# Kernel optimization log

Hardware: AMD Instinct MI355X
Metric: run time of the kernel (lower is better)

Reference implementation:

```python
import jax, jax.numpy as jnp
import numpy as np

SLIDING_WINDOW = 2048
NUM_SINK = 4


def make_mask(q_len, k_len, dtype=jnp.float32):
    # positions of queries in the key axis
    q_pos = jnp.arange(k_len - q_len, k_len)[:, None]  # [Q,1]
    k_pos = jnp.arange(k_len)[None, :]                 # [1,K]
    causal = k_pos <= q_pos
    in_window = k_pos >= (q_pos - SLIDING_WINDOW + 1)
    is_sink = k_pos < NUM_SINK
    allowed = causal & (in_window | is_sink)
    return jnp.where(allowed, jnp.zeros((), dtype), jnp.full((), -jnp.inf, dtype))


def setup_inputs() -> dict:
    key = jax.random.key(0)
    k1, k2, k3 = jax.random.split(key, 3)
    B, H, L, D = 2, 16, 4096, 128
    q = jax.random.normal(k1, (B, H, L, D), dtype=jnp.float32)
    k = jax.random.normal(k2, (B, H, L, D), dtype=jnp.float32)
    v = jax.random.normal(k3, (B, H, L, D), dtype=jnp.float32)
    return {"q": q, "k": k, "v": v}


def reference(q, k, v):
    B, H, L, D = q.shape
    mask = make_mask(L, k.shape[2], q.dtype)  # [L, L] additive
    scale = 1.0 / jnp.sqrt(jnp.asarray(D, q.dtype))
    scores = jnp.einsum('bhqd,bhkd->bhqk', q, k) * scale + mask
    probs = jax.nn.softmax(scores, axis=-1)
    return jnp.einsum('bhqk,bhkd->bhqd', probs, v)
```

## Files before the change

kernel.cpp:

```cpp
#include <hip/hip_runtime.h>

constexpr int Ld = 4096;
constexpr int Dd = 128;
constexpr int BQ = 128;
constexpr int BK = 64;
constexpr int WSZ = 2048;
constexpr int NSINK = 4;
constexpr float QSCALE = 0.08838834764831845f * 1.4426950408889634f;

typedef short bf16x8 __attribute__((ext_vector_type(8)));
typedef float f32x4 __attribute__((ext_vector_type(4)));

#if defined(__has_builtin)
#if __has_builtin(__builtin_amdgcn_exp2f)
#define EXP2(x) __builtin_amdgcn_exp2f(x)
#endif
#endif
#ifndef EXP2
#define EXP2(x) exp2f(x)
#endif

__device__ __forceinline__ unsigned pkbf(float hi, float lo) {
    unsigned r;
    asm("v_cvt_pk_bf16_f32 %0, %1, %2" : "=v"(r) : "v"(lo), "v"(hi));
    return r;
}

__device__ __forceinline__ int rd_off(int row, int d) {
    return row * 128 + ((((d >> 3) ^ row) & 15) << 3) + (d & 7);
}
__device__ __forceinline__ int vt_off(int drow, int key) {
    return drow * 64 + ((((key >> 3) ^ drow) & 7) << 3) + (key & 7);
}
__device__ __forceinline__ int p_off(int row, int key) {
    return row * 64 + ((((key >> 2) ^ ((row & 7) << 1)) & 15) << 2) + (key & 3);
}

typedef const __attribute__((address_space(1))) unsigned int* gas1_t;
typedef __attribute__((address_space(3))) unsigned int* las3_t;
__device__ __forceinline__ void lds16(const void* g, void* l) {
    __builtin_amdgcn_global_load_lds((gas1_t)g, (las3_t)l, 16, 0, 0);
}

__global__ __launch_bounds__(256)
void cvt_kv(const float* __restrict__ Kg, const float* __restrict__ Vg,
            unsigned short* __restrict__ Kw, unsigned short* __restrict__ Vw) {
    __shared__ __align__(16) unsigned short vt[8192];
    const int tid = threadIdx.x;
    const int kb = blockIdx.x * BK;
    const int bh = blockIdx.y;
    const size_t gbase = ((size_t)bh * Ld + kb) * Dd;

    #pragma unroll
    for (int i = 0; i < 8; ++i) {
        int id = tid + i * 256;
        int row = id >> 5;
        int d0 = (id & 31) << 2;
        float4 a = *(const float4*)(Kg + gbase + (size_t)row * Dd + d0);
        *(uint2*)&Kw[gbase + rd_off(row, d0)] =
            make_uint2(pkbf(a.y, a.x), pkbf(a.w, a.z));
    }

    const int vd  = tid & 127;
    const int vkh = tid >> 7;
    const float* vp = Vg + gbase + (size_t)vkh * 32 * Dd + vd;
    float vr[32];
    #pragma unroll
    for (int j = 0; j < 32; ++j) vr[j] = vp[(size_t)j * Dd];
    #pragma unroll
    for (int m2 = 0; m2 < 4; ++m2)
        *(uint4*)&vt[vt_off(vd, vkh * 32 + m2 * 8)] =
            make_uint4(pkbf(vr[m2 * 8 + 1], vr[m2 * 8 + 0]),
                       pkbf(vr[m2 * 8 + 3], vr[m2 * 8 + 2]),
                       pkbf(vr[m2 * 8 + 5], vr[m2 * 8 + 4]),
                       pkbf(vr[m2 * 8 + 7], vr[m2 * 8 + 6]));
    __syncthreads();
    const size_t vbase = ((size_t)bh * (Ld / BK) + blockIdx.x) * (size_t)(BK * Dd);
    #pragma unroll
    for (int i = 0; i < 4; ++i) {
        int j = tid + i * 256;
        *(uint4*)&Vw[vbase + (size_t)j * 8] = *(const uint4*)&vt[j * 8];
    }
}

__global__ __launch_bounds__(256, 3)
void swa_fwd2(const float* __restrict__ Qg, const unsigned short* __restrict__ Kw,
              const unsigned short* __restrict__ Vw, float* __restrict__ Og) {
    __shared__ __align__(16) unsigned short smem[24576];
    unsigned short* Vts = smem + 8192;
    unsigned short* Ps  = smem + 16384;
    unsigned short* Qst = smem;

    const int tid  = threadIdx.x;
    const int w    = tid >> 6;
    const int lane = tid & 63;
    const int ml   = lane & 15;
    const int quad = lane >> 4;

    const unsigned wgr = blockIdx.x;
    const unsigned nwg = gridDim.x;
    unsigned wgid = wgr;
    if ((nwg & 7u) == 0u) wgid = (wgr & 7u) * (nwg >> 3) + (wgr >> 3);
    const int tpb   = Ld / BQ;
    const int bh    = (int)(wgid / (unsigned)tpb);
    const int qtile = tpb - 1 - (int)(wgid % (unsigned)tpb);
    const int q0 = qtile * BQ;

    const size_t baseQ = ((size_t)bh * Ld + q0) * Dd;

    #pragma unroll
    for (int i = 0; i < 16; ++i) {
        int idx = tid + i * 256;
        int row = idx >> 5;
        int d0  = (idx & 31) << 2;
        float4 v = *(const float4*)(Qg + baseQ + (size_t)row * Dd + d0);
        *(uint2*)&Qst[rd_off(row, d0)] =
            make_uint2(pkbf(v.y * QSCALE, v.x * QSCALE),
                       pkbf(v.w * QSCALE, v.z * QSCALE));
    }
    __syncthreads();

    bf16x8 qf[2][4];
    #pragma unroll
    for (int g = 0; g < 2; ++g)
        #pragma unroll
        for (int k0 = 0; k0 < 4; ++k0)
            qf[g][k0] = *(const bf16x8*)&Qst[rd_off(w * 32 + g * 16 + ml,
                                                    k0 * 32 + quad * 8)];
    __syncthreads();

    float l_i[2] = {0.f, 0.f};
    f32x4 o_acc[2][8];
    #pragma unroll
    for (int g = 0; g < 2; ++g)
        #pragma unroll
        for (int dt = 0; dt < 8; ++dt)
            o_acc[g][dt] = (f32x4){0.f, 0.f, 0.f, 0.f};

    const int kmin = (q0 - (WSZ - 1)) > 0 ? (q0 - (WSZ - 1)) : 0;
    const int kb_first = (kmin / BK) * BK;
    const bool sink_extra = (kb_first > 0);
    const int nch = (q0 + BQ - kb_first) / BK + (sink_extra ? 1 : 0);

    const int qrow0 = q0 + w * 32 + ml;
    unsigned short* Pw = Ps + w * 2048;

    auto kb_of = [&](int ci) {
        return sink_extra ? (ci == 0 ? 0 : kb_first + (ci - 1) * BK)
                          : kb_first + ci * BK;
    };
    const size_t kwbase = (size_t)bh * Ld * Dd;
    const size_t vwbase = (size_t)bh * (Ld / BK) * (size_t)(BK * Dd);

    auto stageK = [&](int ci) {
        const int kb = kb_of(ci);
        const unsigned short* kg = Kw + kwbase + (size_t)kb * Dd + tid * 8;
        unsigned short* kl = smem + tid * 8;
        #pragma unroll
        for (int i = 0; i < 4; ++i) lds16(kg + i * 2048, kl + i * 2048);
    };
    auto stageV = [&](int ci) {
        const int kb = kb_of(ci);
        const unsigned short* vg = Vw + vwbase + (size_t)(kb >> 6) * (BK * Dd) + tid * 8;
        unsigned short* vl = Vts + tid * 8;
        #pragma unroll
        for (int i = 0; i < 4; ++i) lds16(vg + i * 2048, vl + i * 2048);
    };

    stageK(0);

    for (int ci = 0; ci < nch; ++ci) {
        __syncthreads();
        stageV(ci);

        const int kb = kb_of(ci);
        const int ck = (ci + 1 < nch) ? ci + 1 : ci;

        f32x4 s[2][4];
        #pragma unroll
        for (int g = 0; g < 2; ++g)
            #pragma unroll
            for (int t = 0; t < 4; ++t)
                s[g][t] = (f32x4){0.f, 0.f, 0.f, 0.f};
        __builtin_amdgcn_s_setprio(1);
        #pragma unroll
        for (int k0 = 0; k0 < 4; ++k0) {
            bf16x8 ka[4];
            #pragma unroll
            for (int t = 0; t < 4; ++t)
                ka[t] = *(const bf16x8*)&smem[rd_off(t * 16 + ml, k0 * 32 + quad * 8)];
            #pragma unroll
            for (int t = 0; t < 4; ++t) {
                s[0][t] = __builtin_amdgcn_mfma_f32_16x16x32_bf16(ka[t], qf[0][k0], s[0][t], 0, 0, 0);
                s[1][t] = __builtin_amdgcn_mfma_f32_16x16x32_bf16(ka[t], qf[1][k0], s[1][t], 0, 0, 0);
            }
        }
        __builtin_amdgcn_s_setprio(0);

        asm volatile("s_waitcnt lgkmcnt(0)" ::: "memory");
        __builtin_amdgcn_sched_barrier(0);
        __builtin_amdgcn_s_barrier();
        stageK(ck);

        const bool full = (kb + (BK - 1) <= q0) && (kb >= q0 + BQ - WSZ);

        #pragma unroll
        for (int g = 0; g < 2; ++g) {
            const int q = qrow0 + g * 16;
            if (!full) {
                #pragma unroll
                for (int t = 0; t < 4; ++t)
                    #pragma unroll
                    for (int r = 0; r < 4; ++r) {
                        int k = kb + t * 16 + quad * 4 + r;
                        bool ok = (k <= q) && ((k + (WSZ - 1) >= q) || (k < NSINK));
                        s[g][t][r] = ok ? s[g][t][r] : -3e38f;
                    }
            }
            float rs = 0.f;
            #pragma unroll
            for (int t = 0; t < 4; ++t)
                #pragma unroll
                for (int r = 0; r < 4; ++r) {
                    float p = EXP2(s[g][t][r]);
                    s[g][t][r] = p;
                    rs += p;
                }
            l_i[g] += rs;

            unsigned short* Pg = Pw + g * 1024;
            #pragma unroll
            for (int t = 0; t < 4; ++t)
                *(uint2*)&Pg[p_off(ml, t * 16 + quad * 4)] =
                    make_uint2(pkbf(s[g][t][1], s[g][t][0]),
                               pkbf(s[g][t][3], s[g][t][2]));
        }

        asm volatile("s_waitcnt vmcnt(4)" ::: "memory");
        __builtin_amdgcn_sched_barrier(0);
        __builtin_amdgcn_s_barrier();

        __builtin_amdgcn_s_setprio(1);
        #pragma unroll
        for (int k0 = 0; k0 < 2; ++k0) {
            bf16x8 pb0 = *(const bf16x8*)&Pw[p_off(ml, k0 * 32 + quad * 8)];
            bf16x8 pb1 = *(const bf16x8*)&Pw[1024 + p_off(ml, k0 * 32 + quad * 8)];
            #pragma unroll
            for (int dt = 0; dt < 8; ++dt) {
                bf16x8 va = *(const bf16x8*)&Vts[vt_off(dt * 16 + ml, k0 * 32 + quad * 8)];
                o_acc[0][dt] = __builtin_amdgcn_mfma_f32_16x16x32_bf16(va, pb0, o_acc[0][dt], 0, 0, 0);
                o_acc[1][dt] = __builtin_amdgcn_mfma_f32_16x16x32_bf16(va, pb1, o_acc[1][dt], 0, 0, 0);
            }
        }
        __builtin_amdgcn_s_setprio(0);
    }

    #pragma unroll
    for (int g = 0; g < 2; ++g) {
        float lt = l_i[g];
        lt += __shfl_xor(lt, 16);
        lt += __shfl_xor(lt, 32);
        const float inv = 1.f / lt;
        float* op = Og + ((size_t)bh * Ld + (qrow0 + g * 16)) * Dd;
        #pragma unroll
        for (int dt = 0; dt < 8; ++dt) {
            float4 o;
            o.x = o_acc[g][dt][0] * inv;
            o.y = o_acc[g][dt][1] * inv;
            o.z = o_acc[g][dt][2] * inv;
            o.w = o_acc[g][dt][3] * inv;
            *(float4*)(op + dt * 16 + quad * 4) = o;
        }
    }
}

__global__ __launch_bounds__(256, 2)
void swa_fwd(const float* __restrict__ Qg, const float* __restrict__ Kg,
             const float* __restrict__ Vg, float* __restrict__ Og) {
    __shared__ __align__(16) unsigned short smem[24576];
    unsigned short* Ks  = smem;
    unsigned short* Vts = smem + 8192;
    unsigned short* Ps  = smem + 16384;
    unsigned short* Qst = smem;

    const int tid  = threadIdx.x;
    const int w    = tid >> 6;
    const int lane = tid & 63;
    const int ml   = lane & 15;
    const int quad = lane >> 4;

    const int qtile = (int)(gridDim.x - 1u - blockIdx.x);
    const int q0 = qtile * BQ;
    const int bh = blockIdx.y;

    const size_t baseQ  = ((size_t)bh * Ld + q0) * Dd;
    const size_t baseKV = (size_t)bh * Ld * Dd;

    #pragma unroll
    for (int i = 0; i < 16; ++i) {
        int idx = tid + i * 256;
        int row = idx >> 5;
        int d0  = (idx & 31) << 2;
        float4 v = *(const float4*)(Qg + baseQ + (size_t)row * Dd + d0);
        *(uint2*)&Qst[rd_off(row, d0)] =
            make_uint2(pkbf(v.y * QSCALE, v.x * QSCALE),
                       pkbf(v.w * QSCALE, v.z * QSCALE));
    }
    __syncthreads();

    bf16x8 qf[2][4];
    #pragma unroll
    for (int g = 0; g < 2; ++g)
        #pragma unroll
        for (int k0 = 0; k0 < 4; ++k0)
            qf[g][k0] = *(const bf16x8*)&Qst[rd_off(w * 32 + g * 16 + ml,
                                                    k0 * 32 + quad * 8)];

    float l_i[2] = {0.f, 0.f};
    f32x4 o_acc[2][8];
    #pragma unroll
    for (int g = 0; g < 2; ++g)
        #pragma unroll
        for (int dt = 0; dt < 8; ++dt)
            o_acc[g][dt] = (f32x4){0.f, 0.f, 0.f, 0.f};

    const int kmin = (q0 - (WSZ - 1)) > 0 ? (q0 - (WSZ - 1)) : 0;
    const int kb_first = (kmin / BK) * BK;
    const bool sink_extra = (kb_first > 0);
    const int nch = (q0 + BQ - kb_first) / BK + (sink_extra ? 1 : 0);

    const int qrow0 = q0 + w * 32 + ml;
    unsigned short* Pw = Ps + w * 2048;

    float4 kreg[8];
    float  vreg[32];
    const int kr0 = tid >> 5;
    const int kd0 = (tid & 31) << 2;
    const int vd  = tid & 127;
    const int vkh = tid >> 7;

    auto kvload = [&](int kb) {
        const float* kp = Kg + baseKV + (size_t)(kb + kr0) * Dd + kd0;
        #pragma unroll
        for (int i = 0; i < 8; ++i)
            kreg[i] = *(const float4*)(kp + (size_t)i * 8 * Dd);
        const float* vp = Vg + baseKV + (size_t)(kb + vkh * 32) * Dd + vd;
        #pragma unroll
        for (int j = 0; j < 32; ++j)
            vreg[j] = vp[(size_t)j * Dd];
    };
    auto kb_of = [&](int ci) {
        return sink_extra ? (ci == 0 ? 0 : kb_first + (ci - 1) * BK)
                          : kb_first + ci * BK;
    };

    kvload(kb_of(0));

    for (int ci = 0; ci < nch; ++ci) {
        const int kb = kb_of(ci);
        __syncthreads();
        #pragma unroll
        for (int i = 0; i < 8; ++i)
            *(uint2*)&Ks[rd_off(kr0 + i * 8, kd0)] =
                make_uint2(pkbf(kreg[i].y, kreg[i].x),
                           pkbf(kreg[i].w, kreg[i].z));
        #pragma unroll
        for (int m2 = 0; m2 < 4; ++m2) {
            *(uint4*)&Vts[vt_off(vd, vkh * 32 + m2 * 8)] =
                make_uint4(pkbf(vreg[m2 * 8 + 1], vreg[m2 * 8 + 0]),
                           pkbf(vreg[m2 * 8 + 3], vreg[m2 * 8 + 2]),
                           pkbf(vreg[m2 * 8 + 5], vreg[m2 * 8 + 4]),
                           pkbf(vreg[m2 * 8 + 7], vreg[m2 * 8 + 6]));
        }
        __syncthreads();
        if (ci + 1 < nch) kvload(kb_of(ci + 1));

        f32x4 s[2][4];
        #pragma unroll
        for (int g = 0; g < 2; ++g)
            #pragma unroll
            for (int t = 0; t < 4; ++t)
                s[g][t] = (f32x4){0.f, 0.f, 0.f, 0.f};
        #pragma unroll
        for (int k0 = 0; k0 < 4; ++k0) {
            bf16x8 ka[4];
            #pragma unroll
            for (int t = 0; t < 4; ++t)
                ka[t] = *(const bf16x8*)&Ks[rd_off(t * 16 + ml, k0 * 32 + quad * 8)];
            #pragma unroll
            for (int t = 0; t < 4; ++t) {
                s[0][t] = __builtin_amdgcn_mfma_f32_16x16x32_bf16(ka[t], qf[0][k0], s[0][t], 0, 0, 0);
                s[1][t] = __builtin_amdgcn_mfma_f32_16x16x32_bf16(ka[t], qf[1][k0], s[1][t], 0, 0, 0);
            }
        }

        const bool full = (kb + (BK - 1) <= q0) && (kb >= q0 + BQ - WSZ);

        #pragma unroll
        for (int g = 0; g < 2; ++g) {
            const int q = qrow0 + g * 16;
            if (!full) {
                #pragma unroll
                for (int t = 0; t < 4; ++t)
                    #pragma unroll
                    for (int r = 0; r < 4; ++r) {
                        int k = kb + t * 16 + quad * 4 + r;
                        bool ok = (k <= q) && ((k + (WSZ - 1) >= q) || (k < NSINK));
                        s[g][t][r] = ok ? s[g][t][r] : -3e38f;
                    }
            }
            float rs = 0.f;
            #pragma unroll
            for (int t = 0; t < 4; ++t)
                #pragma unroll
                for (int r = 0; r < 4; ++r) {
                    float p = EXP2(s[g][t][r]);
                    s[g][t][r] = p;
                    rs += p;
                }
            l_i[g] += rs;

            unsigned short* Pg = Pw + g * 1024;
            #pragma unroll
            for (int t = 0; t < 4; ++t)
                *(uint2*)&Pg[p_off(ml, t * 16 + quad * 4)] =
                    make_uint2(pkbf(s[g][t][1], s[g][t][0]),
                               pkbf(s[g][t][3], s[g][t][2]));
        }

        #pragma unroll
        for (int k0 = 0; k0 < 2; ++k0) {
            bf16x8 pb0 = *(const bf16x8*)&Pw[p_off(ml, k0 * 32 + quad * 8)];
            bf16x8 pb1 = *(const bf16x8*)&Pw[1024 + p_off(ml, k0 * 32 + quad * 8)];
            #pragma unroll
            for (int dt = 0; dt < 8; ++dt) {
                bf16x8 va = *(const bf16x8*)&Vts[vt_off(dt * 16 + ml, k0 * 32 + quad * 8)];
                o_acc[0][dt] = __builtin_amdgcn_mfma_f32_16x16x32_bf16(va, pb0, o_acc[0][dt], 0, 0, 0);
                o_acc[1][dt] = __builtin_amdgcn_mfma_f32_16x16x32_bf16(va, pb1, o_acc[1][dt], 0, 0, 0);
            }
        }
    }

    #pragma unroll
    for (int g = 0; g < 2; ++g) {
        float lt = l_i[g];
        lt += __shfl_xor(lt, 16);
        lt += __shfl_xor(lt, 32);
        const float inv = 1.f / lt;
        float* op = Og + ((size_t)bh * Ld + (qrow0 + g * 16)) * Dd;
        #pragma unroll
        for (int dt = 0; dt < 8; ++dt) {
            float4 o;
            o.x = o_acc[g][dt][0] * inv;
            o.y = o_acc[g][dt][1] * inv;
            o.z = o_acc[g][dt][2] * inv;
            o.w = o_acc[g][dt][3] * inv;
            *(float4*)(op + dt * 16 + quad * 4) = o;
        }
    }
}

extern "C" void kernel_launch(void* const* d_in, const int* in_sizes, int n_in,
                              void* d_out, int out_size, void* d_ws, size_t ws_size,
                              hipStream_t stream) {
    const float* q = (const float*)d_in[0];
    const float* k = (const float*)d_in[1];
    const float* v = (const float*)d_in[2];
    float* o = (float*)d_out;
    const int bhn = in_sizes[0] / (Ld * Dd);
    const size_t elems = (size_t)bhn * Ld * Dd;
    const size_t need = 2 * elems * sizeof(unsigned short);
    if (d_ws != nullptr && ws_size >= need) {
        unsigned short* Kw = (unsigned short*)d_ws;
        unsigned short* Vw = Kw + elems;
        cvt_kv<<<dim3(Ld / BK, bhn), dim3(256, 1, 1), 0, stream>>>(k, v, Kw, Vw);
        swa_fwd2<<<dim3((unsigned)(bhn * (Ld / BQ))), dim3(256, 1, 1), 0, stream>>>(q, Kw, Vw, o);
    } else {
        dim3 grid(Ld / BQ, bhn);
        swa_fwd<<<grid, dim3(256, 1, 1), 0, stream>>>(q, k, v, o);
    }
}
```

Measured before the change: 351.2 us.

## Process 128-key chunks per iteration with two-half QK/PV interleave

Doubles the key chunk handled per loop iteration from 64 to 128 keys. The V-conversion kernel now writes V in a 128-key transposed, swizzled layout, and LDS grows to hold 128-key K and V tiles. Each iteration computes QK and softmax for two 64-key halves, then runs two PV passes, which halves the number of barrier and staging rounds. In exchange, LDS use rises, occupancy drops from 3 to 2 blocks per CU, and the sink chunk wastes half of a 128-key load.

```diff
diff --git a/kernel.cpp b/kernel.cpp
--- a/kernel.cpp
+++ b/kernel.cpp
@@ -4,6 +4,7 @@
 constexpr int Dd = 128;
 constexpr int BQ = 128;
 constexpr int BK = 64;
+constexpr int CHK = 128;
 constexpr int WSZ = 2048;
 constexpr int NSINK = 4;
 constexpr float QSCALE = 0.08838834764831845f * 1.4426950408889634f;
@@ -29,8 +30,11 @@
 __device__ __forceinline__ int rd_off(int row, int d) {
     return row * 128 + ((((d >> 3) ^ row) & 15) << 3) + (d & 7);
 }
-__device__ __forceinline__ int vt_off(int drow, int key) {
+__device__ __forceinline__ int vt64(int drow, int key) {
     return drow * 64 + ((((key >> 3) ^ drow) & 7) << 3) + (key & 7);
+}
+__device__ __forceinline__ int vt128(int drow, int key) {
+    return drow * 128 + ((((key >> 3) ^ drow) & 15) << 3) + (key & 7);
 }
 __device__ __forceinline__ int p_off(int row, int key) {
     return row * 64 + ((((key >> 2) ^ ((row & 7) << 1)) & 15) << 2) + (key & 3);
@@ -69,26 +73,32 @@
     for (int j = 0; j < 32; ++j) vr[j] = vp[(size_t)j * Dd];
     #pragma unroll
     for (int m2 = 0; m2 < 4; ++m2)
-        *(uint4*)&vt[vt_off(vd, vkh * 32 + m2 * 8)] =
+        *(uint4*)&vt[vt64(vd, vkh * 32 + m2 * 8)] =
             make_uint4(pkbf(vr[m2 * 8 + 1], vr[m2 * 8 + 0]),
                        pkbf(vr[m2 * 8 + 3], vr[m2 * 8 + 2]),
                        pkbf(vr[m2 * 8 + 5], vr[m2 * 8 + 4]),
                        pkbf(vr[m2 * 8 + 7], vr[m2 * 8 + 6]));
     __syncthreads();
-    const size_t vbase = ((size_t)bh * (Ld / BK) + blockIdx.x) * (size_t)(BK * Dd);
+    const int t128 = kb >> 7;
+    const int khalf = (kb >> 6) & 1;
+    const size_t vbase = (size_t)bh * Ld * Dd + (size_t)t128 * (CHK * Dd);
     #pragma unroll
     for (int i = 0; i < 4; ++i) {
         int j = tid + i * 256;
-        *(uint4*)&Vw[vbase + (size_t)j * 8] = *(const uint4*)&vt[j * 8];
-    }
-}
-
-__global__ __launch_bounds__(256, 3)
+        int d = j >> 3;
+        int kb8 = j & 7;
+        *(uint4*)&Vw[vbase + d * 128 +
+                     ((((khalf * 8 + kb8) ^ d) & 15) << 3)] =
+            *(const uint4*)&vt[vt64(d, kb8 * 8)];
+    }
+}
+
+__global__ __launch_bounds__(256, 2)
 void swa_fwd2(const float* __restrict__ Qg, const unsigned short* __restrict__ Kw,
               const unsigned short* __restrict__ Vw, float* __restrict__ Og) {
-    __shared__ __align__(16) unsigned short smem[24576];
-    unsigned short* Vts = smem + 8192;
-    unsigned short* Ps  = smem + 16384;
+    __shared__ __align__(16) unsigned short smem[40960];
+    unsigned short* Vts = smem + 16384;
+    unsigned short* Ps  = smem + 32768;
     unsigned short* Qst = smem;
 
     const int tid  = threadIdx.x;
@@ -138,45 +148,36 @@
             o_acc[g][dt] = (f32x4){0.f, 0.f, 0.f, 0.f};
 
     const int kmin = (q0 - (WSZ - 1)) > 0 ? (q0 - (WSZ - 1)) : 0;
-    const int kb_first = (kmin / BK) * BK;
+    const int kb_first = (kmin / CHK) * CHK;
     const bool sink_extra = (kb_first > 0);
-    const int nch = (q0 + BQ - kb_first) / BK + (sink_extra ? 1 : 0);
+    const int nch = (q0 + BQ - kb_first) / CHK + (sink_extra ? 1 : 0);
 
     const int qrow0 = q0 + w * 32 + ml;
     unsigned short* Pw = Ps + w * 2048;
 
     auto kb_of = [&](int ci) {
-        return sink_extra ? (ci == 0 ? 0 : kb_first + (ci - 1) * BK)
-                          : kb_first + ci * BK;
+        return sink_extra ? (ci == 0 ? 0 : kb_first + (ci - 1) * CHK)
+                          : kb_first + ci * CHK;
     };
     const size_t kwbase = (size_t)bh * Ld * Dd;
-    const size_t vwbase = (size_t)bh * (Ld / BK) * (size_t)(BK * Dd);
+    const size_t vwbase = (size_t)bh * Ld * Dd;
 
     auto stageK = [&](int ci) {
         const int kb = kb_of(ci);
         const unsigned short* kg = Kw + kwbase + (size_t)kb * Dd + tid * 8;
         unsigned short* kl = smem + tid * 8;
         #pragma unroll
-        for (int i = 0; i < 4; ++i) lds16(kg + i * 2048, kl + i * 2048);
+        for (int i = 0; i < 8; ++i) lds16(kg + i * 2048, kl + i * 2048);
     };
     auto stageV = [&](int ci) {
         const int kb = kb_of(ci);
-        const unsigned short* vg = Vw + vwbase + (size_t)(kb >> 6) * (BK * Dd) + tid * 8;
+        const unsigned short* vg = Vw + vwbase + (size_t)(kb >> 7) * (CHK * Dd) + tid * 8;
         unsigned short* vl = Vts + tid * 8;
         #pragma unroll
-        for (int i = 0; i < 4; ++i) lds16(vg + i * 2048, vl + i * 2048);
-    };
-
-    stageK(0);
-
-    for (int ci = 0; ci < nch; ++ci) {
-        __syncthreads();
-        stageV(ci);
-
-        const int kb = kb_of(ci);
-        const int ck = (ci + 1 < nch) ? ci + 1 : ci;
-
-        f32x4 s[2][4];
+        for (int i = 0; i < 8; ++i) lds16(vg + i * 2048, vl + i * 2048);
+    };
+
+    auto qk_half = [&](int h, f32x4 (&s)[2][4]) {
         #pragma unroll
         for (int g = 0; g < 2; ++g)
             #pragma unroll
@@ -188,7 +189,8 @@
             bf16x8 ka[4];
             #pragma unroll
             for (int t = 0; t < 4; ++t)
-                ka[t] = *(const bf16x8*)&smem[rd_off(t * 16 + ml, k0 * 32 + quad * 8)];
+                ka[t] = *(const bf16x8*)&smem[rd_off(h * 64 + t * 16 + ml,
+                                                     k0 * 32 + quad * 8)];
             #pragma unroll
             for (int t = 0; t < 4; ++t) {
                 s[0][t] = __builtin_amdgcn_mfma_f32_16x16x32_bf16(ka[t], qf[0][k0], s[0][t], 0, 0, 0);
@@ -196,11 +198,239 @@
             }
         }
         __builtin_amdgcn_s_setprio(0);
+    };
+
+    auto softmax_half = [&](int h, int kb, f32x4 (&s)[2][4]) {
+        const bool fullh = (kb + h * 64 + 63 <= q0) &&
+                           (kb + h * 64 >= q0 + BQ - WSZ);
+        #pragma unroll
+        for (int g = 0; g < 2; ++g) {
+            const int q = qrow0 + g * 16;
+            if (!fullh) {
+                #pragma unroll
+                for (int t = 0; t < 4; ++t)
+                    #pragma unroll
+                    for (int r = 0; r < 4; ++r) {
+                        int k = kb + h * 64 + t * 16 + quad * 4 + r;
+                        bool ok = (k <= q) && ((k + (WSZ - 1) >= q) || (k < NSINK));
+                        s[g][t][r] = ok ? s[g][t][r] : -3e38f;
+                    }
+            }
+            float rs = 0.f;
+            #pragma unroll
+            for (int t = 0; t < 4; ++t)
+                #pragma unroll
+                for (int r = 0; r < 4; ++r) {
+                    float p = EXP2(s[g][t][r]);
+                    s[g][t][r] = p;
+                    rs += p;
+                }
+            l_i[g] += rs;
+        }
+    };
+
+    auto storeP = [&](f32x4 (&s)[2][4]) {
+        #pragma unroll
+        for (int g = 0; g < 2; ++g) {
+            unsigned short* Pg = Pw + g * 1024;
+            #pragma unroll
+            for (int t = 0; t < 4; ++t)
+                *(uint2*)&Pg[p_off(ml, t * 16 + quad * 4)] =
+                    make_uint2(pkbf(s[g][t][1], s[g][t][0]),
+                               pkbf(s[g][t][3], s[g][t][2]));
+        }
+    };
+
+    auto pv_half = [&](int h) {
+        __builtin_amdgcn_s_setprio(1);
+        #pragma unroll
+        for (int k0 = 0; k0 < 2; ++k0) {
+            bf16x8 pb0 = *(const bf16x8*)&Pw[p_off(ml, k0 * 32 + quad * 8)];
+            bf16x8 pb1 = *(const bf16x8*)&Pw[1024 + p_off(ml, k0 * 32 + quad * 8)];
+            #pragma unroll
+            for (int dt = 0; dt < 8; ++dt) {
+                bf16x8 va = *(const bf16x8*)&Vts[vt128(dt * 16 + ml,
+                                                       h * 64 + k0 * 32 + quad * 8)];
+                o_acc[0][dt] = __builtin_amdgcn_mfma_f32_16x16x32_bf16(va, pb0, o_acc[0][dt], 0, 0, 0);
+                o_acc[1][dt] = __builtin_amdgcn_mfma_f32_16x16x32_bf16(va, pb1, o_acc[1][dt], 0, 0, 0);
+            }
+        }
+        __builtin_amdgcn_s_setprio(0);
+    };
+
+    stageK(0);
+
+    for (int ci = 0; ci < nch; ++ci) {
+        __syncthreads();
+        stageV(ci);
+
+        const int kb = kb_of(ci);
+        const int ck = (ci + 1 < nch) ? ci + 1 : ci;
+        const bool sinkch = sink_extra && (ci == 0);
+
+        f32x4 s0[2][4], s1[2][4];
+        qk_half(0, s0);
+        softmax_half(0, kb, s0);
+        storeP(s0);
+        if (!sinkch) {
+            qk_half(1, s1);
+            softmax_half(1, kb, s1);
+        }
 
         asm volatile("s_waitcnt lgkmcnt(0)" ::: "memory");
         __builtin_amdgcn_sched_barrier(0);
         __builtin_amdgcn_s_barrier();
         stageK(ck);
+
+        asm volatile("s_waitcnt vmcnt(8)" ::: "memory");
+        __builtin_amdgcn_sched_barrier(0);
+        __builtin_amdgcn_s_barrier();
+
+        pv_half(0);
+        if (!sinkch) {
+            storeP(s1);
+            pv_half(1);
+        }
+    }
+
+    #pragma unroll
+    for (int g = 0; g < 2; ++g) {
+        float lt = l_i[g];
+        lt += __shfl_xor(lt, 16);
+        lt += __shfl_xor(lt, 32);
+        const float inv = 1.f / lt;
+        float* op = Og + ((size_t)bh * Ld + (qrow0 + g * 16)) * Dd;
+        #pragma unroll
+        for (int dt = 0; dt < 8; ++dt) {
+            float4 o;
+            o.x = o_acc[g][dt][0] * inv;
+            o.y = o_acc[g][dt][1] * inv;
+            o.z = o_acc[g][dt][2] * inv;
+            o.w = o_acc[g][dt][3] * inv;
+            *(float4*)(op + dt * 16 + quad * 4) = o;
+        }
+    }
+}
+
+__global__ __launch_bounds__(256, 2)
+void swa_fwd(const float* __restrict__ Qg, const float* __restrict__ Kg,
+             const float* __restrict__ Vg, float* __restrict__ Og) {
+    __shared__ __align__(16) unsigned short smem[24576];
+    unsigned short* Ks  = smem;
+    unsigned short* Vts = smem + 8192;
+    unsigned short* Ps  = smem + 16384;
+    unsigned short* Qst = smem;
+
+    const int tid  = threadIdx.x;
+    const int w    = tid >> 6;
+    const int lane = tid & 63;
+    const int ml   = lane & 15;
+    const int quad = lane >> 4;
+
+    const int qtile = (int)(gridDim.x - 1u - blockIdx.x);
+    const int q0 = qtile * BQ;
+    const int bh = blockIdx.y;
+
+    const size_t baseQ  = ((size_t)bh * Ld + q0) * Dd;
+    const size_t baseKV = (size_t)bh * Ld * Dd;
+
+    #pragma unroll
+    for (int i = 0; i < 16; ++i) {
+        int idx = tid + i * 256;
+        int row = idx >> 5;
+        int d0  = (idx & 31) << 2;
+        float4 v = *(const float4*)(Qg + baseQ + (size_t)row * Dd + d0);
+        *(uint2*)&Qst[rd_off(row, d0)] =
+            make_uint2(pkbf(v.y * QSCALE, v.x * QSCALE),
+                       pkbf(v.w * QSCALE, v.z * QSCALE));
+    }
+    __syncthreads();
+
+    bf16x8 qf[2][4];
+    #pragma unroll
+    for (int g = 0; g < 2; ++g)
+        #pragma unroll
+        for (int k0 = 0; k0 < 4; ++k0)
+            qf[g][k0] = *(const bf16x8*)&Qst[rd_off(w * 32 + g * 16 + ml,
+                                                    k0 * 32 + quad * 8)];
+
+    float l_i[2] = {0.f, 0.f};
+    f32x4 o_acc[2][8];
+    #pragma unroll
+    for (int g = 0; g < 2; ++g)
+        #pragma unroll
+        for (int dt = 0; dt < 8; ++dt)
+            o_acc[g][dt] = (f32x4){0.f, 0.f, 0.f, 0.f};
+
+    const int kmin = (q0 - (WSZ - 1)) > 0 ? (q0 - (WSZ - 1)) : 0;
+    const int kb_first = (kmin / BK) * BK;
+    const bool sink_extra = (kb_first > 0);
+    const int nch = (q0 + BQ - kb_first) / BK + (sink_extra ? 1 : 0);
+
+    const int qrow0 = q0 + w * 32 + ml;
+    unsigned short* Pw = Ps + w * 2048;
+
+    float4 kreg[8];
+    float  vreg[32];
+    const int kr0 = tid >> 5;
+    const int kd0 = (tid & 31) << 2;
+    const int vd  = tid & 127;
+    const int vkh = tid >> 7;
+
+    auto kvload = [&](int kb) {
+        const float* kp = Kg + baseKV + (size_t)(kb + kr0) * Dd + kd0;
+        #pragma unroll
+        for (int i = 0; i < 8; ++i)
+            kreg[i] = *(const float4*)(kp + (size_t)i * 8 * Dd);
+        const float* vp = Vg + baseKV + (size_t)(kb + vkh * 32) * Dd + vd;
+        #pragma unroll
+        for (int j = 0; j < 32; ++j)
+            vreg[j] = vp[(size_t)j * Dd];
+    };
+    auto kb_of = [&](int ci) {
+        return sink_extra ? (ci == 0 ? 0 : kb_first + (ci - 1) * BK)
+                          : kb_first + ci * BK;
+    };
+
+    kvload(kb_of(0));
+
+    for (int ci = 0; ci < nch; ++ci) {
+        const int kb = kb_of(ci);
+        __syncthreads();
+        #pragma unroll
+        for (int i = 0; i < 8; ++i)
+            *(uint2*)&Ks[rd_off(kr0 + i * 8, kd0)] =
+                make_uint2(pkbf(kreg[i].y, kreg[i].x),
+                           pkbf(kreg[i].w, kreg[i].z));
+        #pragma unroll
+        for (int m2 = 0; m2 < 4; ++m2) {
+            *(uint4*)&Vts[vt64(vd, vkh * 32 + m2 * 8)] =
+                make_uint4(pkbf(vreg[m2 * 8 + 1], vreg[m2 * 8 + 0]),
+                           pkbf(vreg[m2 * 8 + 3], vreg[m2 * 8 + 2]),
+                           pkbf(vreg[m2 * 8 + 5], vreg[m2 * 8 + 4]),
+                           pkbf(vreg[m2 * 8 + 7], vreg[m2 * 8 + 6]));
+        }
+        __syncthreads();
+        if (ci + 1 < nch) kvload(kb_of(ci + 1));
+
+        f32x4 s[2][4];
+        #pragma unroll
+        for (int g = 0; g < 2; ++g)
+            #pragma unroll
+            for (int t = 0; t < 4; ++t)
+                s[g][t] = (f32x4){0.f, 0.f, 0.f, 0.f};
+        #pragma unroll
+        for (int k0 = 0; k0 < 4; ++k0) {
+            bf16x8 ka[4];
+            #pragma unroll
+            for (int t = 0; t < 4; ++t)
+                ka[t] = *(const bf16x8*)&Ks[rd_off(t * 16 + ml, k0 * 32 + quad * 8)];
+            #pragma unroll
+            for (int t = 0; t < 4; ++t) {
+                s[0][t] = __builtin_amdgcn_mfma_f32_16x16x32_bf16(ka[t], qf[0][k0], s[0][t], 0, 0, 0);
+                s[1][t] = __builtin_amdgcn_mfma_f32_16x16x32_bf16(ka[t], qf[1][k0], s[1][t], 0, 0, 0);
+            }
+        }
 
         const bool full = (kb + (BK - 1) <= q0) && (kb >= q0 + BQ - WSZ);
 
@@ -236,205 +466,13 @@
                                pkbf(s[g][t][3], s[g][t][2]));
         }
 
-        asm volatile("s_waitcnt vmcnt(4)" ::: "memory");
-        __builtin_amdgcn_sched_barrier(0);
-        __builtin_amdgcn_s_barrier();
-
-        __builtin_amdgcn_s_setprio(1);
         #pragma unroll
         for (int k0 = 0; k0 < 2; ++k0) {
             bf16x8 pb0 = *(const bf16x8*)&Pw[p_off(ml, k0 * 32 + quad * 8)];
             bf16x8 pb1 = *(const bf16x8*)&Pw[1024 + p_off(ml, k0 * 32 + quad * 8)];
             #pragma unroll
             for (int dt = 0; dt < 8; ++dt) {
-                bf16x8 va = *(const bf16x8*)&Vts[vt_off(dt * 16 + ml, k0 * 32 + quad * 8)];
-                o_acc[0][dt] = __builtin_amdgcn_mfma_f32_16x16x32_bf16(va, pb0, o_acc[0][dt], 0, 0, 0);
-                o_acc[1][dt] = __builtin_amdgcn_mfma_f32_16x16x32_bf16(va, pb1, o_acc[1][dt], 0, 0, 0);
-            }
-        }
-        __builtin_amdgcn_s_setprio(0);
-    }
-
-    #pragma unroll
-    for (int g = 0; g < 2; ++g) {
-        float lt = l_i[g];
-        lt += __shfl_xor(lt, 16);
-        lt += __shfl_xor(lt, 32);
-        const float inv = 1.f / lt;
-        float* op = Og + ((size_t)bh * Ld + (qrow0 + g * 16)) * Dd;
-        #pragma unroll
-        for (int dt = 0; dt < 8; ++dt) {
-            float4 o;
-            o.x = o_acc[g][dt][0] * inv;
-            o.y = o_acc[g][dt][1] * inv;
-            o.z = o_acc[g][dt][2] * inv;
-            o.w = o_acc[g][dt][3] * inv;
-            *(float4*)(op + dt * 16 + quad * 4) = o;
-        }
-    }
-}
-
-__global__ __launch_bounds__(256, 2)
-void swa_fwd(const float* __restrict__ Qg, const float* __restrict__ Kg,
-             const float* __restrict__ Vg, float* __restrict__ Og) {
-    __shared__ __align__(16) unsigned short smem[24576];
-    unsigned short* Ks  = smem;
-    unsigned short* Vts = smem + 8192;
-    unsigned short* Ps  = smem + 16384;
-    unsigned short* Qst = smem;
-
-    const int tid  = threadIdx.x;
-    const int w    = tid >> 6;
-    const int lane = tid & 63;
-    const int ml   = lane & 15;
-    const int quad = lane >> 4;
-
-    const int qtile = (int)(gridDim.x - 1u - blockIdx.x);
-    const int q0 = qtile * BQ;
-    const int bh = blockIdx.y;
-
-    const size_t baseQ  = ((size_t)bh * Ld + q0) * Dd;
-    const size_t baseKV = (size_t)bh * Ld * Dd;
-
-    #pragma unroll
-    for (int i = 0; i < 16; ++i) {
-        int idx = tid + i * 256;
-        int row = idx >> 5;
-        int d0  = (idx & 31) << 2;
-        float4 v = *(const float4*)(Qg + baseQ + (size_t)row * Dd + d0);
-        *(uint2*)&Qst[rd_off(row, d0)] =
-            make_uint2(pkbf(v.y * QSCALE, v.x * QSCALE),
-                       pkbf(v.w * QSCALE, v.z * QSCALE));
-    }
-    __syncthreads();
-
-    bf16x8 qf[2][4];
-    #pragma unroll
-    for (int g = 0; g < 2; ++g)
-        #pragma unroll
-        for (int k0 = 0; k0 < 4; ++k0)
-            qf[g][k0] = *(const bf16x8*)&Qst[rd_off(w * 32 + g * 16 + ml,
-                                                    k0 * 32 + quad * 8)];
-
-    float l_i[2] = {0.f, 0.f};
-    f32x4 o_acc[2][8];
-    #pragma unroll
-    for (int g = 0; g < 2; ++g)
-        #pragma unroll
-        for (int dt = 0; dt < 8; ++dt)
-            o_acc[g][dt] = (f32x4){0.f, 0.f, 0.f, 0.f};
-
-    const int kmin = (q0 - (WSZ - 1)) > 0 ? (q0 - (WSZ - 1)) : 0;
-    const int kb_first = (kmin / BK) * BK;
-    const bool sink_extra = (kb_first > 0);
-    const int nch = (q0 + BQ - kb_first) / BK + (sink_extra ? 1 : 0);
-
-    const int qrow0 = q0 + w * 32 + ml;
-    unsigned short* Pw = Ps + w * 2048;
-
-    float4 kreg[8];
-    float  vreg[32];
-    const int kr0 = tid >> 5;
-    const int kd0 = (tid & 31) << 2;
-    const int vd  = tid & 127;
-    const int vkh = tid >> 7;
-
-    auto kvload = [&](int kb) {
-        const float* kp = Kg + baseKV + (size_t)(kb + kr0) * Dd + kd0;
-        #pragma unroll
-        for (int i = 0; i < 8; ++i)
-            kreg[i] = *(const float4*)(kp + (size_t)i * 8 * Dd);
-        const float* vp = Vg + baseKV + (size_t)(kb + vkh * 32) * Dd + vd;
-        #pragma unroll
-        for (int j = 0; j < 32; ++j)
-            vreg[j] = vp[(size_t)j * Dd];
-    };
-    auto kb_of = [&](int ci) {
-        return sink_extra ? (ci == 0 ? 0 : kb_first + (ci - 1) * BK)
-                          : kb_first + ci * BK;
-    };
-
-    kvload(kb_of(0));
-
-    for (int ci = 0; ci < nch; ++ci) {
-        const int kb = kb_of(ci);
-        __syncthreads();
-        #pragma unroll
-        for (int i = 0; i < 8; ++i)
-            *(uint2*)&Ks[rd_off(kr0 + i * 8, kd0)] =
-                make_uint2(pkbf(kreg[i].y, kreg[i].x),
-                           pkbf(kreg[i].w, kreg[i].z));
-        #pragma unroll
-        for (int m2 = 0; m2 < 4; ++m2) {
-            *(uint4*)&Vts[vt_off(vd, vkh * 32 + m2 * 8)] =
-                make_uint4(pkbf(vreg[m2 * 8 + 1], vreg[m2 * 8 + 0]),
-                           pkbf(vreg[m2 * 8 + 3], vreg[m2 * 8 + 2]),
-                           pkbf(vreg[m2 * 8 + 5], vreg[m2 * 8 + 4]),
-                           pkbf(vreg[m2 * 8 + 7], vreg[m2 * 8 + 6]));
-        }
-        __syncthreads();
-        if (ci + 1 < nch) kvload(kb_of(ci + 1));
-
-        f32x4 s[2][4];
-        #pragma unroll
-        for (int g = 0; g < 2; ++g)
-            #pragma unroll
-            for (int t = 0; t < 4; ++t)
-                s[g][t] = (f32x4){0.f, 0.f, 0.f, 0.f};
-        #pragma unroll
-        for (int k0 = 0; k0 < 4; ++k0) {
-            bf16x8 ka[4];
-            #pragma unroll
-            for (int t = 0; t < 4; ++t)
-                ka[t] = *(const bf16x8*)&Ks[rd_off(t * 16 + ml, k0 * 32 + quad * 8)];
-            #pragma unroll
-            for (int t = 0; t < 4; ++t) {
-                s[0][t] = __builtin_amdgcn_mfma_f32_16x16x32_bf16(ka[t], qf[0][k0], s[0][t], 0, 0, 0);
-                s[1][t] = __builtin_amdgcn_mfma_f32_16x16x32_bf16(ka[t], qf[1][k0], s[1][t], 0, 0, 0);
-            }
-        }
-
-        const bool full = (kb + (BK - 1) <= q0) && (kb >= q0 + BQ - WSZ);
-
-        #pragma unroll
-        for (int g = 0; g < 2; ++g) {
-            const int q = qrow0 + g * 16;
-            if (!full) {
-                #pragma unroll
-                for (int t = 0; t < 4; ++t)
-                    #pragma unroll
-                    for (int r = 0; r < 4; ++r) {
-                        int k = kb + t * 16 + quad * 4 + r;
-                        bool ok = (k <= q) && ((k + (WSZ - 1) >= q) || (k < NSINK));
-                        s[g][t][r] = ok ? s[g][t][r] : -3e38f;
-                    }
-            }
-            float rs = 0.f;
-            #pragma unroll
-            for (int t = 0; t < 4; ++t)
-                #pragma unroll
-                for (int r = 0; r < 4; ++r) {
-                    float p = EXP2(s[g][t][r]);
-                    s[g][t][r] = p;
-                    rs += p;
-                }
-            l_i[g] += rs;
-
-            unsigned short* Pg = Pw + g * 1024;
-            #pragma unroll
-            for (int t = 0; t < 4; ++t)
-                *(uint2*)&Pg[p_off(ml, t * 16 + quad * 4)] =
-                    make_uint2(pkbf(s[g][t][1], s[g][t][0]),
-                               pkbf(s[g][t][3], s[g][t][2]));
-        }
-
-        #pragma unroll
-        for (int k0 = 0; k0 < 2; ++k0) {
-            bf16x8 pb0 = *(const bf16x8*)&Pw[p_off(ml, k0 * 32 + quad * 8)];
-            bf16x8 pb1 = *(const bf16x8*)&Pw[1024 + p_off(ml, k0 * 32 + quad * 8)];
-            #pragma unroll
-            for (int dt = 0; dt < 8; ++dt) {
-                bf16x8 va = *(const bf16x8*)&Vts[vt_off(dt * 16 + ml, k0 * 32 + quad * 8)];
+                bf16x8 va = *(const bf16x8*)&Vts[vt64(dt * 16 + ml, k0 * 32 + quad * 8)];
                 o_acc[0][dt] = __builtin_amdgcn_mfma_f32_16x16x32_bf16(va, pb0, o_acc[0][dt], 0, 0, 0);
                 o_acc[1][dt] = __builtin_amdgcn_mfma_f32_16x16x32_bf16(va, pb1, o_acc[1][dt], 0, 0, 0);
             }
```

New measurement: 347.5 us. No clear change (-1.1%).
